# Kernel tuning notes

Measured on AMD Instinct MI355X. Metric: run time of the kernel, lower is better.

The kernel has to match this reference:

```python
import jax, jax.numpy as jnp
import numpy as np

B, N, T, W, H, ED, S, C, E = 16, 256, 64, 12, 64, 64, 5, 4, 2048
ALPHA = 1.0
FG = W + H  # gcn_in_channels = window_size + tgcn_hidden_dim


def setup_inputs() -> dict:
    key = jax.random.key(0)
    ks = jax.random.split(key, 26)
    rn = lambda k, shape: jax.random.normal(k, shape, jnp.float32) * 0.1
    x = jax.random.normal(ks[0], (B, N, T), jnp.float32)
    src = jax.random.randint(ks[1], (E,), 0, N)
    off = jax.random.randint(ks[2], (E,), 1, N)
    dst = (src + off) % N  # no self loops
    return {
        'x': x,
        'static_edge_weight': jax.random.uniform(ks[3], (E,), jnp.float32),
        'gsl_gconv_w': rn(ks[4], (FG, ED)), 'gsl_gconv_b': rn(ks[5], (ED,)),
        'gsl_w1': rn(ks[6], (ED, ED)), 'gsl_b1': rn(ks[7], (ED,)),
        'gsl_w2': rn(ks[8], (ED, ED)), 'gsl_b2': rn(ks[9], (ED,)),
        'wz_c': rn(ks[10], (1, H)), 'bz_c': rn(ks[11], (H,)),
        'wz_l': rn(ks[12], (2 * H, H)), 'bz_l': rn(ks[13], (H,)),
        'wr_c': rn(ks[14], (1, H)), 'br_c': rn(ks[15], (H,)),
        'wr_l': rn(ks[16], (2 * H, H)), 'br_l': rn(ks[17], (H,)),
        'wh_c': rn(ks[18], (1, H)), 'bh_c': rn(ks[19], (H,)),
        'wh_l': rn(ks[20], (2 * H, H)), 'bh_l': rn(ks[21], (H,)),
        'cls_w': rn(ks[22], (N * H, C)), 'cls_b': rn(ks[23], (C,)),
        'static_edge_index': jnp.stack([src, dst]).astype(jnp.int32),
    }


def _normalize(A):
    # GCN sym-norm with added self loops; A has zero diagonal by construction.
    Ahat = A + jnp.eye(N, dtype=A.dtype)
    deg = Ahat.sum(axis=-2)  # in-degree (PyG gcn_norm scatters weight on col)
    dinv = jnp.where(deg > 0, 1.0 / jnp.sqrt(deg), 0.0)
    return dinv[..., :, None] * Ahat * dinv[..., None, :]


def reference(x, static_edge_weight, gsl_gconv_w, gsl_gconv_b, gsl_w1, gsl_b1,
              gsl_w2, gsl_b2, wz_c, bz_c, wz_l, bz_l, wr_c, br_c, wr_l, br_l,
              wh_c, bh_c, wh_l, bh_l, cls_w, cls_b, static_edge_index):
    A_stat = jnp.zeros((N, N), jnp.float32).at[static_edge_index[0], static_edge_index[1]].add(static_edge_weight)
    An_stat = _normalize(A_stat)  # [N,N]

    # Sliding windows, left-padded with zeros to window_size W.
    xp = jnp.pad(x, ((0, 0), (0, 0), (W - 1, 0)))
    widx = jnp.arange(T)[:, None] + jnp.arange(W)[None, :]
    wins = jnp.transpose(xp[:, :, widx], (2, 0, 1, 3))      # [T,B,N,W]
    xts = jnp.transpose(x, (2, 0, 1))[..., None]            # [T,B,N,1]
    cnts = jnp.minimum(jnp.arange(T) + 1, S).astype(jnp.float32)
    idxs = jnp.arange(T) % S

    def gcn_s(X, Wm, b):  # static graph, out[j] = sum_i Anorm[i,j] (XW)[i]
        return jnp.einsum('ij,bif->bjf', An_stat, X @ Wm) + b

    def gcn_d(An, X, Wm, b):  # per-batch dynamic graph
        return jnp.einsum('bij,bif->bjf', An, X @ Wm) + b

    def step(carry, xs):
        h, Eh = carry
        win, xt, cnt, idx = xs
        It = jnp.concatenate([win, h], axis=-1)             # [B,N,W+H]
        df = gcn_s(It, gsl_gconv_w, gsl_gconv_b)
        de1 = jnp.tanh(ALPHA * (df @ gsl_w1 + gsl_b1))
        de2 = jnp.tanh(ALPHA * (df @ gsl_w2 + gsl_b2))
        M12 = jnp.einsum('bie,bje->bij', de1, de2)          # de1 @ de2^T
        Et = jax.nn.relu(jnp.tanh(ALPHA * (M12 - jnp.swapaxes(M12, -1, -2))))
        Eh = Eh.at[:, idx].set(Et)                          # ring buffer write
        Mt = Eh.sum(axis=1) / cnt                           # mean over filled slots
        An = _normalize(Mt)
        cz = gcn_d(An, xt, wz_c, bz_c)
        z = jax.nn.sigmoid(jnp.concatenate([cz, h], -1) @ wz_l + bz_l)
        cr = gcn_d(An, xt, wr_c, br_c)
        r = jax.nn.sigmoid(jnp.concatenate([cr, h], -1) @ wr_l + br_l)
        ch = gcn_d(An, xt, wh_c, bh_c)
        ht = jnp.tanh(jnp.concatenate([ch, h * r], -1) @ wh_l + bh_l)
        h = z * h + (1.0 - z) * ht
        return (h, Eh), None

    h0 = jnp.zeros((B, N, H), jnp.float32)
    Eh0 = jnp.zeros((B, S, N, N), jnp.float32)
    (hT, _), _ = jax.lax.scan(step, (h0, Eh0), (wins, xts, cnts, idxs))
    return hT.reshape(B, N * H) @ cls_w + cls_b
```

## Files before the change

kernel.cpp:

```cpp
#include <hip/hip_runtime.h>
#include <hip/hip_bf16.h>


typedef unsigned short u16;
typedef unsigned int u32;
typedef unsigned long long u64;
typedef __attribute__((ext_vector_type(8))) short bf16x8;
typedef __attribute__((ext_vector_type(4))) float f32x4;

#define B_ 16
#define N_ 256
#define T_ 64
#define W_ 12
#define S_ 5
#define E_ 2048
#define G_ 16

__device__ __forceinline__ float b2f(u16 u) {
  union { u32 i; float f; } v; v.i = ((u32)u) << 16; return v.f;
}
__device__ __forceinline__ u16 f2b(float f) {
  union { float f; u32 i; } v; v.f = f;
  u32 x = v.i; x += 0x7fff + ((x >> 16) & 1); return (u16)(x >> 16);
}
__device__ __forceinline__ float ftanh(float x) {
  float e = __expf(-2.f * fabsf(x));
  float t = (1.f - e) / (1.f + e);
  return x < 0.f ? -t : t;
}
__device__ __forceinline__ float fsigm(float x) { return 1.f / (1.f + __expf(-x)); }
__device__ __forceinline__ float cvload(const void* p, size_t i, int f) {
  return f ? ((const float*)p)[i] : b2f(((const u16*)p)[i]);
}
__device__ __forceinline__ u16 cvloadb(const void* p, size_t i, int f) {
  return f ? f2b(((const float*)p)[i]) : ((const u16*)p)[i];
}
__device__ __forceinline__ float gld(const float* p) {
  return __hip_atomic_load(p, __ATOMIC_RELAXED, __HIP_MEMORY_SCOPE_SYSTEM);
}
__device__ __forceinline__ void gst(float* p, float v) {
  __hip_atomic_store(p, v, __ATOMIC_RELAXED, __HIP_MEMORY_SCOPE_SYSTEM);
}
__device__ __forceinline__ u64 gld64(const u64* p) {
  return __hip_atomic_load(p, __ATOMIC_RELAXED, __HIP_MEMORY_SCOPE_SYSTEM);
}
__device__ __forceinline__ void gst64(u64* p, u64 v) {
  __hip_atomic_store(p, v, __ATOMIC_RELAXED, __HIP_MEMORY_SCOPE_SYSTEM);
}
__device__ __forceinline__ u32 gldu(const u32* p) {
  return __hip_atomic_load(p, __ATOMIC_RELAXED, __HIP_MEMORY_SCOPE_SYSTEM);
}
__device__ __forceinline__ f32x4 mfma16(bf16x8 a, bf16x8 b, f32x4 c) {
  return __builtin_amdgcn_mfma_f32_16x16x32_bf16(a, b, c, 0, 0, 0);
}
__device__ __forceinline__ bf16x8 ldfrag(const u16* p) { return *(const bf16x8*)p; }

struct Params {
  const void *x0, *ew0, *gw0, *gb0, *w10, *b10, *w20, *b20;
  const void *wzc0, *bzc0, *wzl0, *bzl0, *wrc0, *brc0, *wrl0, *brl0;
  const void *whc0, *bhc0, *whl0, *bhl0, *clsw0, *clsb0;
  const int* eidx;
  float *degsum, *Eh, *clspart;
  u64 *de1g, *de2g, *xTp, *hgpT;
  u32 *tags;
  void* out;
};

__device__ __forceinline__ void wtag(const u32* tg, u32 target) {
  const int k = threadIdx.x & 15;
  while (!__all((int)(gldu(&tg[k]) >= target)))
    __builtin_amdgcn_s_sleep(1);
}
__device__ __forceinline__ void wtag8(const u32* tg, int base, u32 target) {
  const int k = base + (threadIdx.x & 7);
  while (!__all((int)(gldu(&tg[k]) >= target)))
    __builtin_amdgcn_s_sleep(1);
}
__device__ __forceinline__ void ptag(u32* tg, int wg, u32 val) {
  if (threadIdx.x == 0)
    __hip_atomic_store(&tg[wg], val, __ATOMIC_RELAXED, __HIP_MEMORY_SCOPE_SYSTEM);
}

__global__ void __launch_bounds__(256) dtgcn_main(Params p) {
  __shared__ __align__(16) u16 s_union[21120];
  __shared__ __align__(16) u16 s_gwF[64 * 104];
  __shared__ __align__(16) u16 s_w1T[64 * 72], s_w2T[64 * 72];
  __shared__ __align__(16) u16 s_gzT[64 * 72], s_grT[64 * 72], s_ghT[64 * 72];
  __shared__ __align__(16) u16 s_antO1[16 * 264], s_antO2[16 * 264];
  __shared__ __align__(16) u16 s_m1[16 * 104];
  __shared__ float s_msum[16 * 257];
  __shared__ __align__(16) u16 s_de1I[16 * 72], s_de2I[16 * 72];
  __shared__ __align__(16) u16 s_hbf[16 * 72];
  __shared__ __align__(16) u16 s_dfhr[16 * 72];
  __shared__ float s_colv[16], s_degacc[16];
  __shared__ float s_y[256], s_dinv[256], s_s[16];
  __shared__ float s_uv[384], s_gb[64], s_b1[64], s_b2[64];
  __shared__ int s_flag;

  const int b = blockIdx.x & 15;
  const int wg = blockIdx.x >> 4;
  const int tid = threadIdx.x;
  const int lane = tid & 63;
  const int wv = tid >> 6;
  const int l = lane & 15;
  const int quad = lane >> 4;
  const int r0 = wg * 16;

  u64* de1g = p.de1g + (size_t)b * N_ * 16;
  u64* de2g = p.de2g + (size_t)b * N_ * 16;
  u64* hgpb = p.hgpT + (size_t)b * 64 * 64;
  u64* xTw  = p.xTp + (size_t)b * 64 * 64;
  const u64* xTb = xTw;
  float* degb = p.degsum + (size_t)b * N_;
  u32* tgDe = p.tags + b * 128;
  u32* tgDg = p.tags + b * 128 + 16;
  u32* tgH  = p.tags + b * 128 + 32;
  u32* tgX  = p.tags + b * 128 + 48;
  u32* tgC  = p.tags + b * 128 + 64;

  if (tid == 0) {
    const u16* q = (const u16*)p.x0;
    int c = 0;
    for (int i = 0; i < 256; ++i) {
      int ex = (q[i] >> 7) & 0xff;
      c += (ex >= 110 && ex <= 135);
    }
    s_flag = (c < 200) ? 1 : 0;
  }
  __syncthreads();
  const int fl = s_flag;

  {
    u16* xs = s_union;
    #pragma unroll
    for (int r = 0; r < 4; ++r) {
      const int tt = wg * 4 + r;
      xs[r * 256 + tid] = f2b(cvload(p.x0, ((size_t)b * N_ + tid) * T_ + tt, fl));
    }
    __syncthreads();
    const int r = tid >> 6, c = tid & 63;
    u64 v = (u64)xs[r * 256 + 4 * c]
          | ((u64)xs[r * 256 + 4 * c + 1] << 16)
          | ((u64)xs[r * 256 + 4 * c + 2] << 32)
          | ((u64)xs[r * 256 + 4 * c + 3] << 48);
    gst64(&xTw[(size_t)(wg * 4 + r) * 64 + c], v);
    __syncthreads();
    ptag(tgX, wg, 1);
  }

  {
    float* s_acol = (float*)s_union;
    float* s_dg   = (float*)s_union + 4096;
    for (int i = tid; i < 4096; i += 256) s_acol[i] = 0.f;
    s_dg[tid] = 0.f;
    __syncthreads();
    for (int e2 = tid; e2 < E_; e2 += 256) {
      const int sN = p.eidx[e2], dN = p.eidx[E_ + e2];
      const float wv2 = cvload(p.ew0, e2, fl);
      atomicAdd(&s_dg[dN], wv2);
      const int dl = dN - r0;
      if (dl >= 0 && dl < 16) atomicAdd(&s_acol[sN * 16 + dl], wv2);
    }
    __syncthreads();
    s_dg[tid] = rsqrtf(1.f + s_dg[tid]);
    __syncthreads();
    for (int idx = tid; idx < 4096; idx += 256) {
      const int jl = idx >> 8, i = idx & 255;
      float a = s_acol[i * 16 + jl] + ((i == r0 + jl) ? 1.f : 0.f);
      float v = s_dg[i] * a * s_dg[r0 + jl];
      u16 hi = f2b(v);
      s_antO1[jl * 264 + i] = hi;
      s_antO2[jl * 264 + i] = f2b(v - b2f(hi));
    }
  }

  for (int idx = tid; idx < 64 * 104; idx += 256) {
    const int ee = idx / 104, k = idx - ee * 104;
    u16 v = 0;
    if (k < 64) v = cvloadb(p.gw0, (12 + k) * 64 + ee, fl);
    else if (k < 76) v = cvloadb(p.gw0, (k - 64) * 64 + ee, fl);
    s_gwF[ee * 104 + k] = v;
  }
  for (int idx = tid; idx < 4096; idx += 256) {
    const int ee = idx >> 6, ff = idx & 63;
    s_w1T[ee * 72 + ff] = cvloadb(p.w10, ff * 64 + ee, fl);
    s_w2T[ee * 72 + ff] = cvloadb(p.w20, ff * 64 + ee, fl);
    s_gzT[ee * 72 + ff] = cvloadb(p.wzl0, 4096 + ff * 64 + ee, fl);
    s_grT[ee * 72 + ff] = cvloadb(p.wrl0, 4096 + ff * 64 + ee, fl);
    s_ghT[ee * 72 + ff] = cvloadb(p.whl0, 4096 + ff * 64 + ee, fl);
  }
  if (tid < 64) {
    const int e2 = tid;
    float uz = 0, vz = 0, ur = 0, vr = 0, uh = 0, vh = 0;
    for (int f = 0; f < 64; ++f) {
      float wz = cvload(p.wzl0, f * 64 + e2, fl);
      float wr = cvload(p.wrl0, f * 64 + e2, fl);
      float wh = cvload(p.whl0, f * 64 + e2, fl);
      uz += cvload(p.wzc0, f, fl) * wz; vz += cvload(p.bzc0, f, fl) * wz;
      ur += cvload(p.wrc0, f, fl) * wr; vr += cvload(p.brc0, f, fl) * wr;
      uh += cvload(p.whc0, f, fl) * wh; vh += cvload(p.bhc0, f, fl) * wh;
    }
    s_uv[0 * 64 + e2] = uz; s_uv[1 * 64 + e2] = vz + cvload(p.bzl0, e2, fl);
    s_uv[2 * 64 + e2] = ur; s_uv[3 * 64 + e2] = vr + cvload(p.brl0, e2, fl);
    s_uv[4 * 64 + e2] = uh; s_uv[5 * 64 + e2] = vh + cvload(p.bhl0, e2, fl);
    s_gb[tid] = cvload(p.gb0, tid, fl);
    s_b1[tid] = cvload(p.b10, tid, fl);
    s_b2[tid] = cvload(p.b20, tid, fl);
  }
  for (int idx = tid; idx < 16 * 257; idx += 256) s_msum[idx] = 0.f;
  for (int idx = tid; idx < 16 * 72; idx += 256) s_hbf[idx] = 0;
  for (int idx = tid; idx < 16 * 104; idx += 256) s_m1[idx] = 0;
  for (int idx = 20064 + tid; idx < 21120; idx += 256) s_union[idx] = 0;
  if (tid < 16) s_degacc[tid] = 0.f;
  __syncthreads();

  u16* s_itT = s_union;
  u16* s_j1  = s_union;
  u16* s_j2  = s_union + 9216;
  float* s_part = (float*)s_union;

  float hreg[4] = {0.f, 0.f, 0.f, 0.f};
  const int e = wv * 16 + l;

  for (int t = 0; t < T_; ++t) {
    {
      if (t == 0) wtag(tgX, 1);
      u64 tw0[2], tw1[2];
      #pragma unroll
      for (int q = 0; q < 2; ++q) {
        const int idx = q * 256 + tid;
        const int row = idx >> 5, c = idx & 31;
        const bool ok = idx < 384;
        const int tx = t - (W_ - 1) + row;
        const bool live = ok && tx >= 0;
        tw0[q] = live ? gld64(&xTb[(size_t)tx * 64 + c]) : 0ull;
        tw1[q] = live ? gld64(&xTb[(size_t)tx * 64 + 32 + c]) : 0ull;
      }
      f32x4 accA[2];
      accA[0] = (f32x4){0.f, 0.f, 0.f, 0.f};
      accA[1] = (f32x4){0.f, 0.f, 0.f, 0.f};
      wtag8(tgH, 0, (u32)t);
      {
        u64 th[8];
        #pragma unroll
        for (int q = 0; q < 8; ++q) {
          const int idx = q * 256 + tid;
          const int row = idx >> 5, c = idx & 31;
          th[q] = gld64(&hgpb[(size_t)row * 64 + c]);
        }
        #pragma unroll
        for (int q = 0; q < 8; ++q) {
          const int idx = q * 256 + tid;
          const int row = idx >> 5, c = idx & 31;
          *(u64*)&s_itT[row * 264 + c * 4] = th[q];
        }
        #pragma unroll
        for (int q = 0; q < 2; ++q) {
          const int idx = q * 256 + tid;
          if (idx < 384) {
            const int row = idx >> 5, c = idx & 31;
            *(u64*)&s_itT[(64 + row) * 264 + c * 4] = tw0[q];
          }
        }
      }
      __syncthreads();
      {
        int ti = 0;
        for (int nt = wv; nt < 5; nt += 4, ++ti) {
          #pragma unroll
          for (int ch = 0; ch < 4; ++ch) {
            const int io = ch * 32 + quad * 8;
            bf16x8 bfr = ldfrag(&s_itT[(nt * 16 + l) * 264 + io]);
            accA[ti] = mfma16(ldfrag(&s_antO1[l * 264 + io]), bfr, accA[ti]);
            accA[ti] = mfma16(ldfrag(&s_antO2[l * 264 + io]), bfr, accA[ti]);
          }
        }
      }
      wtag8(tgH, 8, (u32)t);
      {
        u64 th[8];
        #pragma unroll
        for (int q = 0; q < 8; ++q) {
          const int idx = q * 256 + tid;
          const int row = idx >> 5, c = idx & 31;
          th[q] = gld64(&hgpb[(size_t)row * 64 + 32 + c]);
        }
        __syncthreads();
        #pragma unroll
        for (int q = 0; q < 8; ++q) {
          const int idx = q * 256 + tid;
          const int row = idx >> 5, c = idx & 31;
          *(u64*)&s_itT[row * 264 + (32 + c) * 4] = th[q];
        }
        #pragma unroll
        for (int q = 0; q < 2; ++q) {
          const int idx = q * 256 + tid;
          if (idx < 384) {
            const int row = idx >> 5, c = idx & 31;
            *(u64*)&s_itT[(64 + row) * 264 + (32 + c) * 4] = tw1[q];
          }
        }
      }
      __syncthreads();
      {
        int ti = 0;
        for (int nt = wv; nt < 5; nt += 4, ++ti) {
          #pragma unroll
          for (int ch = 4; ch < 8; ++ch) {
            const int io = ch * 32 + quad * 8;
            bf16x8 bfr = ldfrag(&s_itT[(nt * 16 + l) * 264 + io]);
            accA[ti] = mfma16(ldfrag(&s_antO1[l * 264 + io]), bfr, accA[ti]);
            accA[ti] = mfma16(ldfrag(&s_antO2[l * 264 + io]), bfr, accA[ti]);
          }
          #pragma unroll
          for (int r = 0; r < 4; ++r)
            s_m1[(quad * 4 + r) * 104 + nt * 16 + l] = f2b(accA[ti][r]);
        }
      }
      __syncthreads();
      {
        f32x4 dfa = {0.f, 0.f, 0.f, 0.f};
        #pragma unroll
        for (int ks = 0; ks < 3; ++ks) {
          bf16x8 afr = ldfrag(&s_m1[l * 104 + ks * 32 + quad * 8]);
          dfa = mfma16(afr, ldfrag(&s_gwF[e * 104 + ks * 32 + quad * 8]), dfa);
        }
        #pragma unroll
        for (int r = 0; r < 4; ++r)
          s_dfhr[(quad * 4 + r) * 72 + e] = f2b(dfa[r] + s_gb[e]);
      }
      __syncthreads();
      {
        f32x4 E1, E2;
        #pragma unroll
        for (int r = 0; r < 4; ++r) { E1[r] = s_b1[e]; E2[r] = s_b2[e]; }
        #pragma unroll
        for (int ks = 0; ks < 2; ++ks) {
          bf16x8 afr = ldfrag(&s_dfhr[l * 72 + ks * 32 + quad * 8]);
          E1 = mfma16(afr, ldfrag(&s_w1T[e * 72 + ks * 32 + quad * 8]), E1);
          E2 = mfma16(afr, ldfrag(&s_w2T[e * 72 + ks * 32 + quad * 8]), E2);
        }
        #pragma unroll
        for (int r = 0; r < 4; ++r) {
          s_de1I[(quad * 4 + r) * 72 + e] = f2b(ftanh(E1[r]));
          s_de2I[(quad * 4 + r) * 72 + e] = f2b(ftanh(E2[r]));
        }
      }
      __syncthreads();
      {
        const int row = tid >> 4, c = tid & 15;
        u64 v1 = *(const u64*)&s_de1I[row * 72 + c * 4];
        u64 v2 = *(const u64*)&s_de2I[row * 72 + c * 4];
        gst64(&de1g[(size_t)(r0 + row) * 16 + c], v1);
        gst64(&de2g[(size_t)(r0 + row) * 16 + c], v2);
      }
      __syncthreads();
      ptag(tgDe, wg, (u32)(t + 1));
    }

    {
      const int sidx = t % S_;
      float* Ehc = p.Eh + (size_t)(b * S_ + sidx) * N_ * N_;
      if (tid < 16) s_colv[tid] = 0.f;
      bf16x8 bq1[2], bq2[2];
      #pragma unroll
      for (int ks = 0; ks < 2; ++ks) {
        bq1[ks] = ldfrag(&s_de1I[l * 72 + ks * 32 + quad * 8]);
        bq2[ks] = ldfrag(&s_de2I[l * 72 + ks * 32 + quad * 8]);
      }
      float dcacc = 0.f;
      for (int jh = 0; jh < 2; ++jh) {
        wtag8(tgDe, jh * 8, (u32)(t + 1));
        u64 t1[8], t2[8];
        #pragma unroll
        for (int q = 0; q < 8; ++q) {
          const int idx = q * 256 + tid;
          const int row = idx >> 4, c = idx & 15;
          t1[q] = gld64(&de1g[(size_t)(jh * 128 + row) * 16 + c]);
          t2[q] = gld64(&de2g[(size_t)(jh * 128 + row) * 16 + c]);
        }
        __syncthreads();
        #pragma unroll
        for (int q = 0; q < 8; ++q) {
          const int idx = q * 256 + tid;
          const int row = idx >> 4, c = idx & 15;
          *(u64*)&s_j1[row * 72 + c * 4] = t1[q];
          *(u64*)&s_j2[row * 72 + c * 4] = t2[q];
        }
        __syncthreads();
        #pragma unroll
        for (int mt2 = 0; mt2 < 2; ++mt2) {
          const int mt = wv * 2 + mt2;
          f32x4 D1 = {0.f, 0.f, 0.f, 0.f}, D2 = {0.f, 0.f, 0.f, 0.f};
          #pragma unroll
          for (int ks = 0; ks < 2; ++ks) {
            bf16x8 a1 = ldfrag(&s_j1[(mt * 16 + l) * 72 + ks * 32 + quad * 8]);
            bf16x8 a2 = ldfrag(&s_j2[(mt * 16 + l) * 72 + ks * 32 + quad * 8]);
            D1 = mfma16(a1, bq2[ks], D1);
            D2 = mfma16(a2, bq1[ks], D2);
          }
          #pragma unroll
          for (int r = 0; r < 4; ++r) {
            const int i = jh * 128 + mt * 16 + quad * 4 + r;
            float d = ftanh(D1[r] - D2[r]);
            float eN = fmaxf(d, 0.f);
            float old = Ehc[(r0 + l) * N_ + i];
            float dd = eN - old;
            Ehc[(r0 + l) * N_ + i] = eN;
            s_msum[l * 257 + i] += dd;
            dcacc += dd;
          }
        }
      }
      dcacc += __shfl_xor(dcacc, 16);
      dcacc += __shfl_xor(dcacc, 32);
      if (lane < 16) atomicAdd(&s_colv[lane], dcacc);
      __syncthreads();
      if (tid < 16) {
        float nd = s_degacc[tid] + s_colv[tid];
        s_degacc[tid] = nd;
        gst(&degb[r0 + tid], nd);
      }
      __syncthreads();
      ptag(tgDg, wg, (u32)(t + 1));
    }

    {
      f32x4 azh = {0.f, 0.f, 0.f, 0.f}, arh = {0.f, 0.f, 0.f, 0.f};
      #pragma unroll
      for (int ks = 0; ks < 2; ++ks) {
        bf16x8 afr = ldfrag(&s_hbf[l * 72 + ks * 32 + quad * 8]);
        azh = mfma16(afr, ldfrag(&s_gzT[e * 72 + ks * 32 + quad * 8]), azh);
        arh = mfma16(afr, ldfrag(&s_grT[e * 72 + ks * 32 + quad * 8]), arh);
      }
      wtag(tgDg, (u32)(t + 1));
      const float cnt = (float)((t + 1 < S_) ? (t + 1) : S_);
      const float invc = 1.f / cnt;
      {
        float dg = 1.f + gld(&degb[tid]) * invc;
        float di = rsqrtf(dg);
        float xv = cvload(p.x0, ((size_t)b * N_ + tid) * T_ + t, fl);
        s_dinv[tid] = di;
        s_y[tid] = di * xv;
      }
      __syncthreads();
      {
        const int jl = tid & 15, c = tid >> 4;
        float part = 0.f;
        #pragma unroll
        for (int k = 0; k < 16; ++k)
          part += s_msum[jl * 257 + c * 16 + k] * s_y[c * 16 + k];
        s_part[c * 16 + jl] = part;
      }
      __syncthreads();
      if (tid < 16) {
        float tot = 0.f;
        for (int k = 0; k < 16; ++k) tot += s_part[k * 16 + tid];
        const int j = r0 + tid;
        s_s[tid] = s_dinv[j] * (tot * invc + s_y[j]);
      }
      __syncthreads();
      float sv[4];
      #pragma unroll
      for (int r = 0; r < 4; ++r) sv[r] = s_s[quad * 4 + r];
      float zz[4], rr2[4];
      #pragma unroll
      for (int r = 0; r < 4; ++r) {
        zz[r]  = fsigm(azh[r] + s_uv[0 * 64 + e] * sv[r] + s_uv[1 * 64 + e]);
        rr2[r] = fsigm(arh[r] + s_uv[2 * 64 + e] * sv[r] + s_uv[3 * 64 + e]);
      }
      #pragma unroll
      for (int r = 0; r < 4; ++r)
        s_dfhr[(quad * 4 + r) * 72 + e] = f2b(hreg[r] * rr2[r]);
      __syncthreads();
      f32x4 ah;
      #pragma unroll
      for (int r = 0; r < 4; ++r) ah[r] = s_uv[4 * 64 + e] * sv[r] + s_uv[5 * 64 + e];
      #pragma unroll
      for (int ks = 0; ks < 2; ++ks) {
        bf16x8 afr = ldfrag(&s_dfhr[l * 72 + ks * 32 + quad * 8]);
        ah = mfma16(afr, ldfrag(&s_ghT[e * 72 + ks * 32 + quad * 8]), ah);
      }
      #pragma unroll
      for (int r = 0; r < 4; ++r) {
        float ht = ftanh(ah[r]);
        hreg[r] = zz[r] * hreg[r] + (1.f - zz[r]) * ht;
      }
      #pragma unroll
      for (int r = 0; r < 4; ++r)
        s_hbf[(quad * 4 + r) * 72 + e] = f2b(hreg[r]);
      __syncthreads();
      {
        const int k = tid >> 2, c4 = tid & 3;
        u64 v = (u64)s_hbf[(c4 * 4 + 0) * 72 + k]
              | ((u64)s_hbf[(c4 * 4 + 1) * 72 + k] << 16)
              | ((u64)s_hbf[(c4 * 4 + 2) * 72 + k] << 32)
              | ((u64)s_hbf[(c4 * 4 + 3) * 72 + k] << 48);
        gst64(&hgpb[(size_t)k * 64 + (r0 >> 2) + c4], v);
      }
      __syncthreads();
      ptag(tgH, wg, (u32)(t + 1));
    }
  }

  {
    float part[4] = {0.f, 0.f, 0.f, 0.f};
    #pragma unroll
    for (int r = 0; r < 4; ++r) {
      const size_t base = ((size_t)(r0 + quad * 4 + r) * 64 + e) * 4;
      #pragma unroll
      for (int c = 0; c < 4; ++c)
        part[c] += hreg[r] * cvload(p.clsw0, base + c, fl);
    }
    #pragma unroll
    for (int c = 0; c < 4; ++c) {
      float v = part[c];
      v += __shfl_xor(v, 1);  v += __shfl_xor(v, 2);
      v += __shfl_xor(v, 4);  v += __shfl_xor(v, 8);
      v += __shfl_xor(v, 16); v += __shfl_xor(v, 32);
      if (lane == 0) s_s[wv * 4 + c] = v;
    }
    __syncthreads();
    if (tid < 4) {
      float tot = s_s[0 + tid] + s_s[4 + tid] + s_s[8 + tid] + s_s[12 + tid];
      gst(&p.clspart[(b * 16 + wg) * 4 + tid], tot);
    }
    __syncthreads();
    ptag(tgC, wg, 1);
    if (wg == 0) {
      wtag(tgC, 1);
      if (tid < 4) {
        float v = 0.f;
        for (int k = 0; k < 16; ++k) v += gld(&p.clspart[(b * 16 + k) * 4 + tid]);
        v += cvload(p.clsb0, tid, fl);
        if (fl) ((float*)p.out)[b * 4 + tid] = v;
        else    ((u16*)p.out)[b * 4 + tid] = f2b(v);
      }
    }
  }
}

extern "C" void kernel_launch(void* const* d_in, const int* in_sizes, int n_in,
                              void* d_out, int out_size, void* d_ws, size_t ws_size,
                              hipStream_t stream) {
  float* w = (float*)d_ws;
  size_t o = 0;
  auto alloc = [&](size_t n) { float* r = w + o; o += (n + 63) & ~(size_t)63; return r; };
  u64* de1g = (u64*)alloc((size_t)B_ * N_ * 32);
  u64* de2g = (u64*)alloc((size_t)B_ * N_ * 32);
  u64* xTp  = (u64*)alloc((size_t)B_ * 64 * 128);
  float* clspart = alloc(B_ * 16 * 4);
  const size_t zero_off = o;
  u64*   hgpT  = (u64*)alloc((size_t)B_ * 64 * 128);
  float* degs  = alloc((size_t)B_ * N_);
  u32*   tags  = (u32*)alloc(B_ * 128);
  float* Eh    = alloc((size_t)B_ * S_ * N_ * N_);
  if (ws_size < o * sizeof(float)) return;

  (void)hipMemsetAsync(w + zero_off, 0, (o - zero_off) * sizeof(float), stream);

  Params p;
  p.x0  = d_in[0];  p.ew0 = d_in[1];
  p.gw0 = d_in[2];  p.gb0 = d_in[3];
  p.w10 = d_in[4];  p.b10 = d_in[5];
  p.w20 = d_in[6];  p.b20 = d_in[7];
  p.wzc0 = d_in[8];  p.bzc0 = d_in[9];  p.wzl0 = d_in[10]; p.bzl0 = d_in[11];
  p.wrc0 = d_in[12]; p.brc0 = d_in[13]; p.wrl0 = d_in[14]; p.brl0 = d_in[15];
  p.whc0 = d_in[16]; p.bhc0 = d_in[17]; p.whl0 = d_in[18]; p.bhl0 = d_in[19];
  p.clsw0 = d_in[20]; p.clsb0 = d_in[21];
  p.eidx = (const int*)d_in[22];
  p.degsum = degs; p.Eh = Eh; p.clspart = clspart;
  p.de1g = de1g; p.de2g = de2g; p.xTp = xTp; p.hgpT = hgpT;
  p.tags = tags; p.out = d_out;

  void* args[] = { &p };
  hipError_t ce = hipLaunchCooperativeKernel((const void*)dtgcn_main,
                                             dim3(B_ * G_), dim3(256), args, 0, stream);
  if (ce != hipSuccess) {
    (void)hipGetLastError();
    dtgcn_main<<<dim3(B_ * G_), dim3(256), 0, stream>>>(p);
  }
}
```

Before: 885.1 us.

## Prefetch h and de tiles earlier, localize Eh layout, shuffle-reduce mix step

Moves the second-half h load and wait before the first MFMA block and prefetches the second de half while computing the first, so global latency overlaps compute. The Eh ring buffer is laid out per workgroup so reads and writes are contiguous, and old values are loaded ahead of the tag wait. The s_part reduction is replaced by a wave-level shuffle reduction, h is stored straight from registers without an extra LDS round trip and sync, and launch_bounds gains a min-blocks hint. Holding prefetched data in registers raises register pressure.

```diff
diff --git a/kernel.cpp b/kernel.cpp
--- a/kernel.cpp
+++ b/kernel.cpp
@@ -81,7 +81,7 @@
     __hip_atomic_store(&tg[wg], val, __ATOMIC_RELAXED, __HIP_MEMORY_SCOPE_SYSTEM);
 }
 
-__global__ void __launch_bounds__(256) dtgcn_main(Params p) {
+__global__ void __launch_bounds__(256, 1) dtgcn_main(Params p) {
   __shared__ __align__(16) u16 s_union[21120];
   __shared__ __align__(16) u16 s_gwF[64 * 104];
   __shared__ __align__(16) u16 s_w1T[64 * 72], s_w2T[64 * 72];
@@ -217,14 +217,15 @@
   u16* s_itT = s_union;
   u16* s_j1  = s_union;
   u16* s_j2  = s_union + 9216;
-  float* s_part = (float*)s_union;
 
   float hreg[4] = {0.f, 0.f, 0.f, 0.f};
   const int e = wv * 16 + l;
 
   for (int t = 0; t < T_; ++t) {
+    float xv;
     {
       if (t == 0) wtag(tgX, 1);
+      xv = cvload(p.x0, ((size_t)b * N_ + tid) * T_ + t, fl);
       u64 tw0[2], tw1[2];
       #pragma unroll
       for (int q = 0; q < 2; ++q) {
@@ -236,9 +237,6 @@
         tw0[q] = live ? gld64(&xTb[(size_t)tx * 64 + c]) : 0ull;
         tw1[q] = live ? gld64(&xTb[(size_t)tx * 64 + 32 + c]) : 0ull;
       }
-      f32x4 accA[2];
-      accA[0] = (f32x4){0.f, 0.f, 0.f, 0.f};
-      accA[1] = (f32x4){0.f, 0.f, 0.f, 0.f};
       wtag8(tgH, 0, (u32)t);
       {
         u64 th[8];
@@ -264,6 +262,17 @@
         }
       }
       __syncthreads();
+      wtag8(tgH, 8, (u32)t);
+      u64 th1[8];
+      #pragma unroll
+      for (int q = 0; q < 8; ++q) {
+        const int idx = q * 256 + tid;
+        const int row = idx >> 5, c = idx & 31;
+        th1[q] = gld64(&hgpb[(size_t)row * 64 + 32 + c]);
+      }
+      f32x4 accA[2];
+      accA[0] = (f32x4){0.f, 0.f, 0.f, 0.f};
+      accA[1] = (f32x4){0.f, 0.f, 0.f, 0.f};
       {
         int ti = 0;
         for (int nt = wv; nt < 5; nt += 4, ++ti) {
@@ -276,29 +285,18 @@
           }
         }
       }
-      wtag8(tgH, 8, (u32)t);
-      {
-        u64 th[8];
-        #pragma unroll
-        for (int q = 0; q < 8; ++q) {
-          const int idx = q * 256 + tid;
+      #pragma unroll
+      for (int q = 0; q < 8; ++q) {
+        const int idx = q * 256 + tid;
+        const int row = idx >> 5, c = idx & 31;
+        *(u64*)&s_itT[row * 264 + (32 + c) * 4] = th1[q];
+      }
+      #pragma unroll
+      for (int q = 0; q < 2; ++q) {
+        const int idx = q * 256 + tid;
+        if (idx < 384) {
           const int row = idx >> 5, c = idx & 31;
-          th[q] = gld64(&hgpb[(size_t)row * 64 + 32 + c]);
-        }
-        __syncthreads();
-        #pragma unroll
-        for (int q = 0; q < 8; ++q) {
-          const int idx = q * 256 + tid;
-          const int row = idx >> 5, c = idx & 31;
-          *(u64*)&s_itT[row * 264 + (32 + c) * 4] = th[q];
-        }
-        #pragma unroll
-        for (int q = 0; q < 2; ++q) {
-          const int idx = q * 256 + tid;
-          if (idx < 384) {
-            const int row = idx >> 5, c = idx & 31;
-            *(u64*)&s_itT[(64 + row) * 264 + (32 + c) * 4] = tw1[q];
-          }
+          *(u64*)&s_itT[(64 + row) * 264 + (32 + c) * 4] = tw1[q];
         }
       }
       __syncthreads();
@@ -360,7 +358,7 @@
 
     {
       const int sidx = t % S_;
-      float* Ehc = p.Eh + (size_t)(b * S_ + sidx) * N_ * N_;
+      float* Ehc = p.Eh + ((size_t)((b * S_ + sidx) * G_ + wg)) * (N_ * 16);
       if (tid < 16) s_colv[tid] = 0.f;
       bf16x8 bq1[2], bq2[2];
       #pragma unroll
@@ -368,48 +366,95 @@
         bq1[ks] = ldfrag(&s_de1I[l * 72 + ks * 32 + quad * 8]);
         bq2[ks] = ldfrag(&s_de2I[l * 72 + ks * 32 + quad * 8]);
       }
+      float old0[2][4], old1[2][4];
+      #pragma unroll
+      for (int mt2 = 0; mt2 < 2; ++mt2) {
+        const int mt = wv * 2 + mt2;
+        #pragma unroll
+        for (int r = 0; r < 4; ++r) {
+          const int i0 = mt * 16 + quad * 4 + r;
+          old0[mt2][r] = Ehc[(size_t)i0 * 16 + l];
+          old1[mt2][r] = Ehc[(size_t)(128 + i0) * 16 + l];
+        }
+      }
+      wtag8(tgDe, 0, (u32)(t + 1));
+      u64 t1a[8], t2a[8];
+      #pragma unroll
+      for (int q = 0; q < 8; ++q) {
+        const int idx = q * 256 + tid;
+        const int row = idx >> 4, c = idx & 15;
+        t1a[q] = gld64(&de1g[(size_t)row * 16 + c]);
+        t2a[q] = gld64(&de2g[(size_t)row * 16 + c]);
+      }
+      #pragma unroll
+      for (int q = 0; q < 8; ++q) {
+        const int idx = q * 256 + tid;
+        const int row = idx >> 4, c = idx & 15;
+        *(u64*)&s_j1[row * 72 + c * 4] = t1a[q];
+        *(u64*)&s_j2[row * 72 + c * 4] = t2a[q];
+      }
+      __syncthreads();
+      wtag8(tgDe, 8, (u32)(t + 1));
+      u64 t1b[8], t2b[8];
+      #pragma unroll
+      for (int q = 0; q < 8; ++q) {
+        const int idx = q * 256 + tid;
+        const int row = idx >> 4, c = idx & 15;
+        t1b[q] = gld64(&de1g[(size_t)(128 + row) * 16 + c]);
+        t2b[q] = gld64(&de2g[(size_t)(128 + row) * 16 + c]);
+      }
       float dcacc = 0.f;
-      for (int jh = 0; jh < 2; ++jh) {
-        wtag8(tgDe, jh * 8, (u32)(t + 1));
-        u64 t1[8], t2[8];
-        #pragma unroll
-        for (int q = 0; q < 8; ++q) {
-          const int idx = q * 256 + tid;
-          const int row = idx >> 4, c = idx & 15;
-          t1[q] = gld64(&de1g[(size_t)(jh * 128 + row) * 16 + c]);
-          t2[q] = gld64(&de2g[(size_t)(jh * 128 + row) * 16 + c]);
-        }
-        __syncthreads();
-        #pragma unroll
-        for (int q = 0; q < 8; ++q) {
-          const int idx = q * 256 + tid;
-          const int row = idx >> 4, c = idx & 15;
-          *(u64*)&s_j1[row * 72 + c * 4] = t1[q];
-          *(u64*)&s_j2[row * 72 + c * 4] = t2[q];
-        }
-        __syncthreads();
-        #pragma unroll
-        for (int mt2 = 0; mt2 < 2; ++mt2) {
-          const int mt = wv * 2 + mt2;
-          f32x4 D1 = {0.f, 0.f, 0.f, 0.f}, D2 = {0.f, 0.f, 0.f, 0.f};
-          #pragma unroll
-          for (int ks = 0; ks < 2; ++ks) {
-            bf16x8 a1 = ldfrag(&s_j1[(mt * 16 + l) * 72 + ks * 32 + quad * 8]);
-            bf16x8 a2 = ldfrag(&s_j2[(mt * 16 + l) * 72 + ks * 32 + quad * 8]);
-            D1 = mfma16(a1, bq2[ks], D1);
-            D2 = mfma16(a2, bq1[ks], D2);
-          }
-          #pragma unroll
-          for (int r = 0; r < 4; ++r) {
-            const int i = jh * 128 + mt * 16 + quad * 4 + r;
-            float d = ftanh(D1[r] - D2[r]);
-            float eN = fmaxf(d, 0.f);
-            float old = Ehc[(r0 + l) * N_ + i];
-            float dd = eN - old;
-            Ehc[(r0 + l) * N_ + i] = eN;
-            s_msum[l * 257 + i] += dd;
-            dcacc += dd;
-          }
+      #pragma unroll
+      for (int mt2 = 0; mt2 < 2; ++mt2) {
+        const int mt = wv * 2 + mt2;
+        f32x4 D1 = {0.f, 0.f, 0.f, 0.f}, D2 = {0.f, 0.f, 0.f, 0.f};
+        #pragma unroll
+        for (int ks = 0; ks < 2; ++ks) {
+          bf16x8 a1 = ldfrag(&s_j1[(mt * 16 + l) * 72 + ks * 32 + quad * 8]);
+          bf16x8 a2 = ldfrag(&s_j2[(mt * 16 + l) * 72 + ks * 32 + quad * 8]);
+          D1 = mfma16(a1, bq2[ks], D1);
+          D2 = mfma16(a2, bq1[ks], D2);
+        }
+        #pragma unroll
+        for (int r = 0; r < 4; ++r) {
+          const int i = mt * 16 + quad * 4 + r;
+          float d = ftanh(D1[r] - D2[r]);
+          float eN = fmaxf(d, 0.f);
+          float dd = eN - old0[mt2][r];
+          Ehc[(size_t)i * 16 + l] = eN;
+          s_msum[l * 257 + i] += dd;
+          dcacc += dd;
+        }
+      }
+      __syncthreads();
+      #pragma unroll
+      for (int q = 0; q < 8; ++q) {
+        const int idx = q * 256 + tid;
+        const int row = idx >> 4, c = idx & 15;
+        *(u64*)&s_j1[row * 72 + c * 4] = t1b[q];
+        *(u64*)&s_j2[row * 72 + c * 4] = t2b[q];
+      }
+      __syncthreads();
+      #pragma unroll
+      for (int mt2 = 0; mt2 < 2; ++mt2) {
+        const int mt = wv * 2 + mt2;
+        f32x4 D1 = {0.f, 0.f, 0.f, 0.f}, D2 = {0.f, 0.f, 0.f, 0.f};
+        #pragma unroll
+        for (int ks = 0; ks < 2; ++ks) {
+          bf16x8 a1 = ldfrag(&s_j1[(mt * 16 + l) * 72 + ks * 32 + quad * 8]);
+          bf16x8 a2 = ldfrag(&s_j2[(mt * 16 + l) * 72 + ks * 32 + quad * 8]);
+          D1 = mfma16(a1, bq2[ks], D1);
+          D2 = mfma16(a2, bq1[ks], D2);
+        }
+        #pragma unroll
+        for (int r = 0; r < 4; ++r) {
+          const int i = 128 + mt * 16 + quad * 4 + r;
+          float d = ftanh(D1[r] - D2[r]);
+          float eN = fmaxf(d, 0.f);
+          float dd = eN - old1[mt2][r];
+          Ehc[(size_t)i * 16 + l] = eN;
+          s_msum[l * 257 + i] += dd;
+          dcacc += dd;
         }
       }
       dcacc += __shfl_xor(dcacc, 16);
@@ -439,25 +484,26 @@
       {
         float dg = 1.f + gld(&degb[tid]) * invc;
         float di = rsqrtf(dg);
-        float xv = cvload(p.x0, ((size_t)b * N_ + tid) * T_ + t, fl);
         s_dinv[tid] = di;
         s_y[tid] = di * xv;
       }
       __syncthreads();
       {
-        const int jl = tid & 15, c = tid >> 4;
+        const int jl = tid >> 4, cc = tid & 15;
         float part = 0.f;
         #pragma unroll
-        for (int k = 0; k < 16; ++k)
-          part += s_msum[jl * 257 + c * 16 + k] * s_y[c * 16 + k];
-        s_part[c * 16 + jl] = part;
-      }
-      __syncthreads();
-      if (tid < 16) {
-        float tot = 0.f;
-        for (int k = 0; k < 16; ++k) tot += s_part[k * 16 + tid];
-        const int j = r0 + tid;
-        s_s[tid] = s_dinv[j] * (tot * invc + s_y[j]);
+        for (int k = 0; k < 16; ++k) {
+          const int i = cc * 16 + ((k + cc) & 15);
+          part += s_msum[jl * 257 + i] * s_y[i];
+        }
+        part += __shfl_xor(part, 1);
+        part += __shfl_xor(part, 2);
+        part += __shfl_xor(part, 4);
+        part += __shfl_xor(part, 8);
+        if (cc == 0) {
+          const int j = r0 + jl;
+          s_s[jl] = s_dinv[j] * (part * invc + s_y[j]);
+        }
       }
       __syncthreads();
       float sv[4];
@@ -486,17 +532,15 @@
         float ht = ftanh(ah[r]);
         hreg[r] = zz[r] * hreg[r] + (1.f - zz[r]) * ht;
       }
-      #pragma unroll
-      for (int r = 0; r < 4; ++r)
-        s_hbf[(quad * 4 + r) * 72 + e] = f2b(hreg[r]);
-      __syncthreads();
-      {
-        const int k = tid >> 2, c4 = tid & 3;
-        u64 v = (u64)s_hbf[(c4 * 4 + 0) * 72 + k]
-              | ((u64)s_hbf[(c4 * 4 + 1) * 72 + k] << 16)
-              | ((u64)s_hbf[(c4 * 4 + 2) * 72 + k] << 32)
-              | ((u64)s_hbf[(c4 * 4 + 3) * 72 + k] << 48);
-        gst64(&hgpb[(size_t)k * 64 + (r0 >> 2) + c4], v);
+      {
+        u16 h0 = f2b(hreg[0]), h1 = f2b(hreg[1]);
+        u16 h2 = f2b(hreg[2]), h3 = f2b(hreg[3]);
+        u64 hv = (u64)h0 | ((u64)h1 << 16) | ((u64)h2 << 32) | ((u64)h3 << 48);
+        gst64(&hgpb[(size_t)e * 64 + (r0 >> 2) + quad], hv);
+        s_hbf[(quad * 4 + 0) * 72 + e] = h0;
+        s_hbf[(quad * 4 + 1) * 72 + e] = h1;
+        s_hbf[(quad * 4 + 2) * 72 + e] = h2;
+        s_hbf[(quad * 4 + 3) * 72 + e] = h3;
       }
       __syncthreads();
       ptag(tgH, wg, (u32)(t + 1));
```

After: 854.4 us. 3.5% less time.
